# Performance work log

Measured on AMD Instinct MI355X. Metric: run time of the kernel, lower is better.

## Reference

```python
import jax, jax.numpy as jnp
import numpy as np

N_NODES = 100000
DIM = 256
N_SAMPLES = 64
N_CLASSES = 10


def setup_inputs() -> dict:
    key = jax.random.key(0)
    k1, k2, k3 = jax.random.split(key, 3)
    data = jax.random.normal(k1, (N_SAMPLES, DIM), dtype=jnp.float32)
    V = jax.random.uniform(k2, (N_NODES, DIM), dtype=jnp.float32)  # node matrix (torch.rand init)
    labels = jax.random.randint(k3, (N_SAMPLES,), 0, N_CLASSES)
    return {"data": data, "V": V, "labels": labels, "it": 0}


def reference(data, V, labels, it):
    # SOINN+ per-sample BMU search + BMU/sBMU weight pull, fixed node capacity.
    # eps schedules exactly as in ASOINN.forward.
    eps_b = 1.0 / (it + 2)
    eps_n = 1.0 / ((it + 1) * 100)

    def step(Vc, sample):
        # pairwise L2 distance of sample vs all nodes: [N]
        diff = sample[None, :] - Vc
        dists = jnp.sqrt(jnp.sum(diff * diff, axis=-1) + 1e-12)
        neg_vals, idx = jax.lax.top_k(-dists, 2)  # two smallest
        b, s = idx[0], idx[1]
        # update_bmu: V[b] += eps_b * (sample - V[b]); neighbor pull on sBMU
        Vc = Vc.at[b].add(eps_b * (sample - Vc[b]))
        Vc = Vc.at[s].add(eps_n * (sample - Vc[s]))
        return Vc, -neg_vals  # (b_dist, s_dist)

    V_final, bmu_dists = jax.lax.scan(step, V, data)
    return bmu_dists  # [N_SAMPLES, 2]
```

## Files before the change

kernel.cpp:

```cpp
#include <hip/hip_runtime.h>
#include <math.h>


#define N_NODES 100000
#define DIM     256
#define NS      64
#define NCH     1563
#define KC      32
#define NBMW    3125
#define CAP     4096
#define KL      192
#define KLS     136

typedef unsigned long long u64;

__device__ __forceinline__ u64 pk(float d, int i) {
  return ((u64)__float_as_uint(d) << 32) | (unsigned)i;
}
__device__ __forceinline__ u64 umin64(u64 a, u64 b) { return a < b ? a : b; }
__device__ __forceinline__ u64 umax64(u64 a, u64 b) { return a > b ? a : b; }
__device__ __forceinline__ void mrg2(u64& A0, u64& A1, u64 B0, u64 B1) {
  u64 m = umax64(A0, B0);
  A0 = umin64(A0, B0);
  A1 = umin64(umin64(A1, B1), m);
}

template <int C>
__device__ __forceinline__ u64 dpp64(u64 x) {
  unsigned lo = (unsigned)__builtin_amdgcn_update_dpp(
      (int)0xFFFFFFFF, (int)(unsigned)(x & 0xFFFFFFFFull), C, 0xF, 0xF, false);
  unsigned hi = (unsigned)__builtin_amdgcn_update_dpp(
      (int)0xFFFFFFFF, (int)(unsigned)(x >> 32), C, 0xF, 0xF, false);
  return ((u64)hi << 32) | lo;
}
template <int C>
__device__ __forceinline__ void dpp_round(u64& A0, u64& A1) {
  u64 B0 = dpp64<C>(A0);
  u64 B1 = dpp64<C>(A1);
  mrg2(A0, A1, B0, B1);
}

__global__ void k_xx(const float* __restrict__ X, float* __restrict__ XX) {
  int i = blockIdx.x, j = threadIdx.x;
  const float* xi = X + i * DIM;
  const float* xj = X + j * DIM;
  float acc = 0.f;
  for (int k = 0; k < DIM; k += 4) {
    float4 a = *(const float4*)(xi + k);
    float4 b = *(const float4*)(xj + k);
    acc += a.x * b.x + a.y * b.y + a.z * b.z + a.w * b.w;
  }
  XX[i * NS + j] = acc;
}

__global__ __launch_bounds__(256) void k_dist(const float* __restrict__ X,
                                              const float* __restrict__ V,
                                              const float* __restrict__ XX,
                                              float* __restrict__ P,
                                              float* __restrict__ PT,
                                              float* __restrict__ Q,
                                              u64* __restrict__ SUMC) {
  __shared__ float Xl[KC][68];
  __shared__ float Vl[KC][132];
  __shared__ float sq[128];
  const int tid = threadIdx.x;
  const int n0  = blockIdx.x * 128;
  const int ty  = tid >> 5;
  const int tx  = tid & 31;
  float acc[8][4];
#pragma unroll
  for (int i = 0; i < 8; i++)
#pragma unroll
    for (int u = 0; u < 4; u++) acc[i][u] = 0.f;
  float qa = 0.f;
  const int xsl = tid & 63;
  const int xkk = (tid >> 6) * 8;
  const int vn  = tid & 127;
  const int vkk = (tid >> 7) * 16;
  const bool vok = (n0 + vn < N_NODES);
  const float* vrow = V + (size_t)(n0 + vn) * DIM + vkk;
  const float* xrow = X + xsl * DIM + xkk;

  float4 xr0, xr1, vr[4];
  xr0 = *(const float4*)(xrow + 0);
  xr1 = *(const float4*)(xrow + 4);
#pragma unroll
  for (int m = 0; m < 4; m++)
    vr[m] = vok ? *(const float4*)(vrow + 4 * m) : make_float4(0.f, 0.f, 0.f, 0.f);

  for (int c = 0; c < 8; c++) {
    __syncthreads();
    Xl[xkk + 0][xsl] = xr0.x; Xl[xkk + 1][xsl] = xr0.y;
    Xl[xkk + 2][xsl] = xr0.z; Xl[xkk + 3][xsl] = xr0.w;
    Xl[xkk + 4][xsl] = xr1.x; Xl[xkk + 5][xsl] = xr1.y;
    Xl[xkk + 6][xsl] = xr1.z; Xl[xkk + 7][xsl] = xr1.w;
#pragma unroll
    for (int m = 0; m < 4; m++) {
      Vl[vkk + 4 * m + 0][vn] = vr[m].x; Vl[vkk + 4 * m + 1][vn] = vr[m].y;
      Vl[vkk + 4 * m + 2][vn] = vr[m].z; Vl[vkk + 4 * m + 3][vn] = vr[m].w;
    }
    __syncthreads();
    if (c + 1 < 8) {
      int kc = (c + 1) * KC;
      xr0 = *(const float4*)(xrow + kc);
      xr1 = *(const float4*)(xrow + kc + 4);
#pragma unroll
      for (int m = 0; m < 4; m++)
        vr[m] = vok ? *(const float4*)(vrow + kc + 4 * m)
                    : make_float4(0.f, 0.f, 0.f, 0.f);
    }
    if (tid < 128) {
      float qq = 0.f;
#pragma unroll 8
      for (int k = 0; k < KC; k++) { float t = Vl[k][tid]; qq += t * t; }
      qa += qq;
    }
#pragma unroll 4
    for (int k = 0; k < KC; k++) {
      float xs[8], vs[4];
      *(float4*)&xs[0] = *(const float4*)&Xl[k][ty * 8];
      *(float4*)&xs[4] = *(const float4*)&Xl[k][ty * 8 + 4];
      *(float4*)&vs[0] = *(const float4*)&Vl[k][tx * 4];
#pragma unroll
      for (int i = 0; i < 8; i++)
#pragma unroll
        for (int u = 0; u < 4; u++) acc[i][u] += xs[i] * vs[u];
    }
  }
  if (tid < 128) sq[tid] = qa;
  __syncthreads();
  if (tid < 128 && n0 + tid < N_NODES) Q[n0 + tid] = qa;
  float qs[4];
  *(float4*)&qs[0] = *(const float4*)&sq[tx * 4];
  const bool full = (n0 + 128) <= N_NODES;
#pragma unroll
  for (int i = 0; i < 8; i++) {
    int s = ty * 8 + i;
    float xn = XX[s * NS + s];
#pragma unroll
    for (int u = 0; u < 4; u++) acc[i][u] = xn - 2.f * acc[i][u] + qs[u];
    float* prow = P + (size_t)s * N_NODES + n0 + tx * 4;
    if (full) {
      *(float4*)(prow) = make_float4(acc[i][0], acc[i][1], acc[i][2], acc[i][3]);
    } else {
#pragma unroll
      for (int u = 0; u < 4; u++) {
        int n = n0 + tx * 4 + u;
        if (n < N_NODES) prow[u] = acc[i][u];
      }
    }
  }
#pragma unroll
  for (int u = 0; u < 4; u++) {
    int n = n0 + tx * 4 + u;
    if (n < N_NODES) {
      float* pt = PT + (size_t)n * NS + ty * 8;
      *(float4*)(pt)     = make_float4(acc[0][u], acc[1][u], acc[2][u], acc[3][u]);
      *(float4*)(pt + 4) = make_float4(acc[4][u], acc[5][u], acc[6][u], acc[7][u]);
    }
  }
#pragma unroll
  for (int i = 0; i < 8; i++) {
    int s = ty * 8 + i;
    u64 key = ~0ull;
#pragma unroll
    for (int u = 0; u < 4; u++) {
      int n = n0 + tx * 4 + u;
      if (n < N_NODES) key = umin64(key, pk(acc[i][u], n));
    }
#pragma unroll
    for (int off = 1; off <= 8; off <<= 1)
      key = umin64(key, (u64)__shfl_xor((unsigned long long)key, off, 64));
    if ((tx & 15) == 0) {
      int chunk = (n0 >> 6) + (tx >> 4);
      if (chunk < NCH) SUMC[(size_t)s * NCH + chunk] = key;
    }
  }
}

__global__ __launch_bounds__(1024) void k_build(const u64* __restrict__ SUMC,
                                                const float* __restrict__ P,
                                                u64* __restrict__ L) {
  __shared__ u64 A[CAP];
  __shared__ u64 Twave[16];
  __shared__ float Tsh;
  __shared__ int cnt;
  const int j = blockIdx.x, tid = threadIdx.x;
  const int w = tid >> 6, l = tid & 63;
  {
    int base = w * 98;
    u64 v0 = (base + l < NCH) ? SUMC[(size_t)j * NCH + base + l] : ~0ull;
    u64 v1 = (l < 34 && base + 64 + l < NCH)
                 ? SUMC[(size_t)j * NCH + base + 64 + l] : ~0ull;
    u64 s9 = ~0ull;
#pragma unroll
    for (int r = 0; r < 9; r++) {
      u64 m = umin64(v0, v1);
#pragma unroll
      for (int off = 1; off <= 32; off <<= 1)
        m = umin64(m, (u64)__shfl_xor((unsigned long long)m, off, 64));
      if (r == 8) { s9 = m; } else {
        if (v0 == m) v0 = ~0ull;
        if (v1 == m) v1 = ~0ull;
      }
    }
    if (l == 0) Twave[w] = s9;
  }
  __syncthreads();
  if (tid == 0) {
    u64 t = 0;
    for (int i = 0; i < 16; i++) t = umax64(t, Twave[i]);
    Tsh = __uint_as_float((unsigned)(t >> 32));
    cnt = 0;
  }
  __syncthreads();
  const float T = Tsh;
  const float* prow = P + (size_t)j * N_NODES;
  for (int n0 = tid * 4; n0 < N_NODES + 3; n0 += 4096) {
    float d[4];
    if (n0 + 3 < N_NODES) {
      float4 p = *(const float4*)(prow + n0);
      d[0] = p.x; d[1] = p.y; d[2] = p.z; d[3] = p.w;
    } else {
#pragma unroll
      for (int e = 0; e < 4; e++)
        d[e] = (n0 + e < N_NODES) ? prow[n0 + e] : INFINITY;
    }
#pragma unroll
    for (int e = 0; e < 4; e++) {
      if (d[e] <= T) {
        int pos = atomicAdd(&cnt, 1);
        if (pos < CAP) A[pos] = pk(d[e], n0 + e);
      }
    }
  }
  __syncthreads();
  int n = cnt; if (n > CAP) n = CAP;
  int M = 256; while (M < n) M <<= 1;
  for (int i = tid; i < M; i += 1024)
    if (i >= n) A[i] = ~0ull;
  __syncthreads();
  for (int k = 2; k <= M; k <<= 1)
    for (int s2 = k >> 1; s2 > 0; s2 >>= 1) {
      for (int i = tid; i < M; i += 1024) {
        int p = i ^ s2;
        if (p > i) {
          u64 a = A[i], b = A[p];
          bool up = ((i & k) == 0);
          if ((a > b) == up) { A[i] = b; A[p] = a; }
        }
      }
      __syncthreads();
    }
  for (int i = tid; i < KLS; i += 1024) L[(size_t)j * KL + i] = A[i];
}

__global__ __launch_bounds__(192) void k_seq(
    const float* __restrict__ PT, const float* __restrict__ Q,
    const float* __restrict__ XXg, const u64* __restrict__ L,
    const int* __restrict__ itp, float* __restrict__ out) {
  __shared__ float XXl[NS * 65];
  __shared__ float g[128][65];
  __shared__ float qv[128];
  __shared__ unsigned int bitmap[NBMW];
  __shared__ int tracked[128];
  __shared__ u64 cand16[NS][16];
  __shared__ float specg[4][6][NS];
  __shared__ float specq[4][6];
  __shared__ int   specid[4][6];
  __shared__ int ready[NS];
  __shared__ int done[NS];

  const int tid = threadIdx.x;
  const int wv = tid >> 6;
  const int lane = tid & 63;

  for (int i = tid; i < NS * NS; i += 192) {
    int r = i >> 6, c = i & 63;
    XXl[r * 65 + c] = XXg[i];
  }
  for (int i = tid; i < NBMW; i += 192) bitmap[i] = 0u;
  for (int i = tid; i < NS; i += 192) { ready[i] = 0; done[i] = 0; }
  __syncthreads();

  const int it = itp[0];
  const float eps_b = 1.0f / (float)(it + 2);
  const float eps_n = 1.0f / (float)((it + 1) * 100);
  const float xdl = XXl[lane * 65 + lane];

  if (wv == 0) {
    int ns = 0;
    int pw0 = -1, pw1 = -1, pw2 = -1, pw3 = -1;
    for (int j = 0; j < NS; j++) {
      while (__hip_atomic_load(&ready[j], __ATOMIC_ACQUIRE,
                               __HIP_MEMORY_SCOPE_WORKGROUP) == 0)
        __builtin_amdgcn_s_sleep(1);
      const int sb = j & 3;
      u64 ck = (lane < 16) ? cand16[j][lane] : ~0ull;
      float sgv[6], sqv[6]; int sid[6];
#pragma unroll
      for (int s = 0; s < 6; s++) {
        sgv[s] = specg[sb][s][lane];
        sid[s] = specid[sb][s];
        sqv[s] = specq[sb][s];
      }
      float gA = g[lane][j], gB = g[lane + 64][j];
      float qvA = qv[lane],  qvB = qv[lane + 64];
      int   tA = tracked[lane], tB = tracked[lane + 64];
      float xrow = XXl[j * 65 + lane];
      float xnj  = XXl[j * 65 + j];
      u64 A0 = ~0ull, A1 = ~0ull;
      {
        int id = (int)(unsigned)(ck & 0xFFFFFFFFull);
        bool ok = (ck != ~0ull) && id != pw0 && id != pw1 && id != pw2 && id != pw3;
        if (ok) { A0 = ck; }
      }
      if (lane < ns)      { float d = xnj - 2.f * gA + qvA; mrg2(A0, A1, pk(d, tA), ~0ull); }
      if (lane + 64 < ns) { float d = xnj - 2.f * gB + qvB; mrg2(A0, A1, pk(d, tB), ~0ull); }
      dpp_round<0x111>(A0, A1);
      dpp_round<0x112>(A0, A1);
      dpp_round<0x114>(A0, A1);
      dpp_round<0x118>(A0, A1);
      dpp_round<0x142>(A0, A1);
      dpp_round<0x143>(A0, A1);
      const int r0 = (int)(unsigned)__builtin_amdgcn_readlane(
          (int)(unsigned)(A0 & 0xFFFFFFFFull), 63);
      const int r1 = (int)(unsigned)__builtin_amdgcn_readlane(
          (int)(unsigned)(A1 & 0xFFFFFFFFull), 63);
      if (lane == 63) {
        float2 o;
        o.x = sqrtf(fmaxf(__uint_as_float((unsigned)(A0 >> 32)), 0.f) + 1e-12f);
        o.y = sqrtf(fmaxf(__uint_as_float((unsigned)(A1 >> 32)), 0.f) + 1e-12f);
        *(float2*)(out + j * 2) = o;
      }
      bool h0a = (lane < ns) && (tA == r0);
      bool h0b = (lane + 64 < ns) && (tB == r0);
      u64 mk0a = __ballot(h0a), mk0b = __ballot(h0b);
      bool new0 = (mk0a | mk0b) == 0ull;
      int sl0 = new0 ? ns
                     : (mk0a ? (__ffsll((unsigned long long)mk0a) - 1)
                             : (64 + __ffsll((unsigned long long)mk0b) - 1));
      bool h1a = (lane < ns) && (tA == r1);
      bool h1b = (lane + 64 < ns) && (tB == r1);
      u64 mk1a = __ballot(h1a), mk1b = __ballot(h1b);
      bool new1 = (mk1a | mk1b) == 0ull;
      int sl1 = new1 ? (ns + (new0 ? 1 : 0))
                     : (mk1a ? (__ffsll((unsigned long long)mk1a) - 1)
                             : (64 + __ffsll((unsigned long long)mk1b) - 1));
      bool hit0 = false, hit1 = false;
      float pv0 = 0.f, qq0 = 0.f, pv1 = 0.f, qq1 = 0.f;
#pragma unroll
      for (int s = 0; s < 6; s++) {
        bool h0 = (sid[s] == r0), h1 = (sid[s] == r1);
        pv0 = h0 ? sgv[s] : pv0;  qq0 = h0 ? sqv[s] : qq0;  hit0 |= h0;
        pv1 = h1 ? sgv[s] : pv1;  qq1 = h1 ? sqv[s] : qq1;  hit1 |= h1;
      }
      if (new0 && !hit0) { pv0 = PT[(size_t)r0 * NS + lane]; qq0 = Q[r0]; }
      if (new1 && !hit1) { pv1 = PT[(size_t)r1 * NS + lane]; qq1 = Q[r1]; }
      float gt0 = g[sl0][lane];
      float gt1 = g[sl1][lane];
      float gold0 = new0 ? (0.5f * (xdl + qq0 - pv0)) : gt0;
      float qold0 = new0 ? qq0
                         : __uint_as_float((unsigned)__builtin_amdgcn_readlane(
                               (int)__float_as_uint(sl0 < 64 ? qvA : qvB), sl0 & 63));
      float gj0 = __uint_as_float(
          (unsigned)__builtin_amdgcn_readlane((int)__float_as_uint(gold0), j));
      g[sl0][lane] = (1.f - eps_b) * gold0 + eps_b * xrow;
      if (lane == 0) {
        float om = 1.f - eps_b;
        qv[sl0] = om * om * qold0 + 2.f * eps_b * om * gj0 + eps_b * eps_b * xnj;
        tracked[sl0] = r0;
        if (new0) bitmap[r0 >> 5] |= 1u << (r0 & 31);
      }
      float gold1 = new1 ? (0.5f * (xdl + qq1 - pv1)) : gt1;
      float qold1 = new1 ? qq1
                         : __uint_as_float((unsigned)__builtin_amdgcn_readlane(
                               (int)__float_as_uint(sl1 < 64 ? qvA : qvB), sl1 & 63));
      float gj1 = __uint_as_float(
          (unsigned)__builtin_amdgcn_readlane((int)__float_as_uint(gold1), j));
      g[sl1][lane] = (1.f - eps_n) * gold1 + eps_n * xrow;
      if (lane == 0) {
        float on = 1.f - eps_n;
        qv[sl1] = on * on * qold1 + 2.f * eps_n * on * gj1 + eps_n * eps_n * xnj;
        tracked[sl1] = r1;
        if (new1) bitmap[r1 >> 5] |= 1u << (r1 & 31);
      }
      ns += (new0 ? 1 : 0) + (new1 ? 1 : 0);
      pw2 = pw0; pw3 = pw1; pw0 = r0; pw1 = r1;
      __hip_atomic_store(&done[j], 1, __ATOMIC_RELEASE,
                         __HIP_MEMORY_SCOPE_WORKGROUP);
    }
  } else {
    for (int t = (wv == 1 ? 0 : 1); t < NS; t += 2) {
      if (t >= 3) {
        while (__hip_atomic_load(&done[t - 3], __ATOMIC_ACQUIRE,
                                 __HIP_MEMORY_SCOPE_WORKGROUP) == 0)
          __builtin_amdgcn_s_sleep(1);
      }
      const u64* Lr = L + (size_t)t * KL;
      u64 e0 = Lr[lane], e1 = Lr[lane + 64];
      u64 e2 = (lane < 8) ? Lr[128 + lane] : ~0ull;
      int i0 = (int)(unsigned)(e0 & 0xFFFFFFFFull);
      int i1 = (int)(unsigned)(e1 & 0xFFFFFFFFull);
      int i2 = (int)(unsigned)(e2 & 0xFFFFFFFFull);
      bool t0 = (e0 == ~0ull) || ((bitmap[i0 >> 5] >> (i0 & 31)) & 1u);
      bool t1 = (e1 == ~0ull) || ((bitmap[i1 >> 5] >> (i1 & 31)) & 1u);
      bool t2 = (e2 == ~0ull) || ((bitmap[i2 >> 5] >> (i2 & 31)) & 1u);
      u64 um0 = ~__ballot(t0), um1 = ~__ballot(t1), um2 = ~__ballot(t2);
      u64 below = (1ull << lane) - 1;
      int c0n = __popcll((unsigned long long)um0);
      int c1n = __popcll((unsigned long long)um1);
      int rank0 = __popcll((unsigned long long)(um0 & below));
      int rank1 = c0n + __popcll((unsigned long long)(um1 & below));
      int rank2 = c0n + c1n + __popcll((unsigned long long)(um2 & below));
      if (!t0 && rank0 < 16) cand16[t][rank0] = e0;
      if (!t1 && rank1 < 16) cand16[t][rank1] = e1;
      if (!t2 && rank2 < 16) cand16[t][rank2] = e2;
      int U = c0n + c1n + __popcll((unsigned long long)um2);
      if (lane < 16 && lane >= U) cand16[t][lane] = ~0ull;
      const int sb = t & 3;
      int ids[6];
#pragma unroll
      for (int s = 0; s < 6; s++)
        ids[s] = (int)(unsigned)(cand16[t][s] & 0xFFFFFFFFull);
#pragma unroll
      for (int s = 0; s < 6; s++)
        specg[sb][s][lane] = PT[(size_t)ids[s] * NS + lane];
      if (lane < 6) {
        specid[sb][lane] = ids[lane];
        specq[sb][lane] = Q[ids[lane]];
      }
      __hip_atomic_store(&ready[t], 1, __ATOMIC_RELEASE,
                         __HIP_MEMORY_SCOPE_WORKGROUP);
    }
  }
}

extern "C" void kernel_launch(void* const* d_in, const int* in_sizes, int n_in,
                              void* d_out, int out_size, void* d_ws, size_t ws_size,
                              hipStream_t stream) {
  const float* X  = (const float*)d_in[0];
  const float* V  = (const float*)d_in[1];
  const int*  itp = (const int*)d_in[3];
  float* out = (float*)d_out;

  char* ws = (char*)d_ws;
  size_t off = 0;
  auto alloc = [&](size_t bytes) -> void* {
    size_t o = (off + 255) & ~(size_t)255;
    off = o + bytes;
    return (void*)(ws + o);
  };
  float* P    = (float*)alloc((size_t)NS * N_NODES * sizeof(float));
  float* PT   = (float*)alloc((size_t)NS * N_NODES * sizeof(float));
  float* Q    = (float*)alloc((size_t)N_NODES * sizeof(float));
  float* XXp  = (float*)alloc((size_t)NS * NS * sizeof(float));
  u64*   SUMC = (u64*)alloc((size_t)NS * NCH * sizeof(u64));
  u64*   Lst  = (u64*)alloc((size_t)NS * KL * sizeof(u64));

  k_xx   <<<NS, NS, 0, stream>>>(X, XXp);
  k_dist <<<(N_NODES + 127) / 128, 256, 0, stream>>>(X, V, XXp, P, PT, Q, SUMC);
  k_build<<<NS, 1024, 0, stream>>>(SUMC, P, Lst);
  k_seq  <<<1, 192, 0, stream>>>(PT, Q, XXp, Lst, itp, out);
}
```

Baseline: 310.2 us.

## Split ready flag, encode tracked slot in key, prefetch candidate list early

The single ready flag becomes two: one signals that the candidate list is published and one signals that the speculative PT rows are loaded. The sequential wave can then start its argmin reduction before the speculative gathers finish. Tracked entries now carry their slot index and a 'tracked' bit in the packed key, so the slot and the new/old status come directly from the reduction result instead of four ballots plus ffs. Helper waves also issue their global loads of the candidate list before waiting on the done flag. Together these shorten the serial critical path, at the cost of an extra spin-wait and the assumption that node ids fit in 17 bits.

Result: no change. 308.1 us (-0.7%).

```diff
diff --git a/kernel.cpp b/kernel.cpp
--- a/kernel.cpp
+++ b/kernel.cpp
@@ -16,6 +16,10 @@
 
 __device__ __forceinline__ u64 pk(float d, int i) {
   return ((u64)__float_as_uint(d) << 32) | (unsigned)i;
+}
+__device__ __forceinline__ u64 tkey(float d, int slot, int node) {
+  return ((u64)__float_as_uint(d) << 32) |
+         (u64)(0x80000000u | ((unsigned)slot << 17) | (unsigned)node);
 }
 __device__ __forceinline__ u64 umin64(u64 a, u64 b) { return a < b ? a : b; }
 __device__ __forceinline__ u64 umax64(u64 a, u64 b) { return a > b ? a : b; }
@@ -268,7 +272,8 @@
   __shared__ float specg[4][6][NS];
   __shared__ float specq[4][6];
   __shared__ int   specid[4][6];
-  __shared__ int ready[NS];
+  __shared__ int readyC[NS];
+  __shared__ int readyS[NS];
   __shared__ int done[NS];
 
   const int tid = threadIdx.x;
@@ -280,7 +285,7 @@
     XXl[r * 65 + c] = XXg[i];
   }
   for (int i = tid; i < NBMW; i += 192) bitmap[i] = 0u;
-  for (int i = tid; i < NS; i += 192) { ready[i] = 0; done[i] = 0; }
+  for (int i = tid; i < NS; i += 192) { readyC[i] = 0; readyS[i] = 0; done[i] = 0; }
   __syncthreads();
 
   const int it = itp[0];
@@ -292,18 +297,11 @@
     int ns = 0;
     int pw0 = -1, pw1 = -1, pw2 = -1, pw3 = -1;
     for (int j = 0; j < NS; j++) {
-      while (__hip_atomic_load(&ready[j], __ATOMIC_ACQUIRE,
+      while (__hip_atomic_load(&readyC[j], __ATOMIC_ACQUIRE,
                                __HIP_MEMORY_SCOPE_WORKGROUP) == 0)
         __builtin_amdgcn_s_sleep(1);
       const int sb = j & 3;
       u64 ck = (lane < 16) ? cand16[j][lane] : ~0ull;
-      float sgv[6], sqv[6]; int sid[6];
-#pragma unroll
-      for (int s = 0; s < 6; s++) {
-        sgv[s] = specg[sb][s][lane];
-        sid[s] = specid[sb][s];
-        sqv[s] = specq[sb][s];
-      }
       float gA = g[lane][j], gB = g[lane + 64][j];
       float qvA = qv[lane],  qvB = qv[lane + 64];
       int   tA = tracked[lane], tB = tracked[lane + 64];
@@ -315,38 +313,42 @@
         bool ok = (ck != ~0ull) && id != pw0 && id != pw1 && id != pw2 && id != pw3;
         if (ok) { A0 = ck; }
       }
-      if (lane < ns)      { float d = xnj - 2.f * gA + qvA; mrg2(A0, A1, pk(d, tA), ~0ull); }
-      if (lane + 64 < ns) { float d = xnj - 2.f * gB + qvB; mrg2(A0, A1, pk(d, tB), ~0ull); }
+      if (lane < ns)      { float d = xnj - 2.f * gA + qvA; mrg2(A0, A1, tkey(d, lane, tA), ~0ull); }
+      if (lane + 64 < ns) { float d = xnj - 2.f * gB + qvB; mrg2(A0, A1, tkey(d, lane + 64, tB), ~0ull); }
       dpp_round<0x111>(A0, A1);
       dpp_round<0x112>(A0, A1);
       dpp_round<0x114>(A0, A1);
       dpp_round<0x118>(A0, A1);
       dpp_round<0x142>(A0, A1);
       dpp_round<0x143>(A0, A1);
-      const int r0 = (int)(unsigned)__builtin_amdgcn_readlane(
+      const unsigned lo0 = (unsigned)__builtin_amdgcn_readlane(
           (int)(unsigned)(A0 & 0xFFFFFFFFull), 63);
-      const int r1 = (int)(unsigned)__builtin_amdgcn_readlane(
+      const unsigned lo1 = (unsigned)__builtin_amdgcn_readlane(
           (int)(unsigned)(A1 & 0xFFFFFFFFull), 63);
+      const int r0 = (int)(lo0 & 0x1FFFFu);
+      const int r1 = (int)(lo1 & 0x1FFFFu);
+      const bool new0 = (lo0 & 0x80000000u) == 0u;
+      const bool new1 = (lo1 & 0x80000000u) == 0u;
+      const int sl0 = new0 ? ns : (int)((lo0 >> 17) & 127u);
+      const int sl1 = new1 ? (ns + (new0 ? 1 : 0)) : (int)((lo1 >> 17) & 127u);
       if (lane == 63) {
         float2 o;
         o.x = sqrtf(fmaxf(__uint_as_float((unsigned)(A0 >> 32)), 0.f) + 1e-12f);
         o.y = sqrtf(fmaxf(__uint_as_float((unsigned)(A1 >> 32)), 0.f) + 1e-12f);
         *(float2*)(out + j * 2) = o;
       }
-      bool h0a = (lane < ns) && (tA == r0);
-      bool h0b = (lane + 64 < ns) && (tB == r0);
-      u64 mk0a = __ballot(h0a), mk0b = __ballot(h0b);
-      bool new0 = (mk0a | mk0b) == 0ull;
-      int sl0 = new0 ? ns
-                     : (mk0a ? (__ffsll((unsigned long long)mk0a) - 1)
-                             : (64 + __ffsll((unsigned long long)mk0b) - 1));
-      bool h1a = (lane < ns) && (tA == r1);
-      bool h1b = (lane + 64 < ns) && (tB == r1);
-      u64 mk1a = __ballot(h1a), mk1b = __ballot(h1b);
-      bool new1 = (mk1a | mk1b) == 0ull;
-      int sl1 = new1 ? (ns + (new0 ? 1 : 0))
-                     : (mk1a ? (__ffsll((unsigned long long)mk1a) - 1)
-                             : (64 + __ffsll((unsigned long long)mk1b) - 1));
+      float gt0 = g[sl0][lane];
+      float gt1 = g[sl1][lane];
+      while (__hip_atomic_load(&readyS[j], __ATOMIC_ACQUIRE,
+                               __HIP_MEMORY_SCOPE_WORKGROUP) == 0)
+        __builtin_amdgcn_s_sleep(1);
+      float sgv[6], sqv[6]; int sid[6];
+#pragma unroll
+      for (int s = 0; s < 6; s++) {
+        sgv[s] = specg[sb][s][lane];
+        sid[s] = specid[sb][s];
+        sqv[s] = specq[sb][s];
+      }
       bool hit0 = false, hit1 = false;
       float pv0 = 0.f, qq0 = 0.f, pv1 = 0.f, qq1 = 0.f;
 #pragma unroll
@@ -357,8 +359,6 @@
       }
       if (new0 && !hit0) { pv0 = PT[(size_t)r0 * NS + lane]; qq0 = Q[r0]; }
       if (new1 && !hit1) { pv1 = PT[(size_t)r1 * NS + lane]; qq1 = Q[r1]; }
-      float gt0 = g[sl0][lane];
-      float gt1 = g[sl1][lane];
       float gold0 = new0 ? (0.5f * (xdl + qq0 - pv0)) : gt0;
       float qold0 = new0 ? qq0
                          : __uint_as_float((unsigned)__builtin_amdgcn_readlane(
@@ -392,14 +392,14 @@
     }
   } else {
     for (int t = (wv == 1 ? 0 : 1); t < NS; t += 2) {
+      const u64* Lr = L + (size_t)t * KL;
+      u64 e0 = Lr[lane], e1 = Lr[lane + 64];
+      u64 e2 = (lane < 8) ? Lr[128 + lane] : ~0ull;
       if (t >= 3) {
         while (__hip_atomic_load(&done[t - 3], __ATOMIC_ACQUIRE,
                                  __HIP_MEMORY_SCOPE_WORKGROUP) == 0)
           __builtin_amdgcn_s_sleep(1);
       }
-      const u64* Lr = L + (size_t)t * KL;
-      u64 e0 = Lr[lane], e1 = Lr[lane + 64];
-      u64 e2 = (lane < 8) ? Lr[128 + lane] : ~0ull;
       int i0 = (int)(unsigned)(e0 & 0xFFFFFFFFull);
       int i1 = (int)(unsigned)(e1 & 0xFFFFFFFFull);
       int i2 = (int)(unsigned)(e2 & 0xFFFFFFFFull);
@@ -418,6 +418,8 @@
       if (!t2 && rank2 < 16) cand16[t][rank2] = e2;
       int U = c0n + c1n + __popcll((unsigned long long)um2);
       if (lane < 16 && lane >= U) cand16[t][lane] = ~0ull;
+      __hip_atomic_store(&readyC[t], 1, __ATOMIC_RELEASE,
+                         __HIP_MEMORY_SCOPE_WORKGROUP);
       const int sb = t & 3;
       int ids[6];
 #pragma unroll
@@ -430,7 +432,7 @@
         specid[sb][lane] = ids[lane];
         specq[sb][lane] = Q[ids[lane]];
       }
-      __hip_atomic_store(&ready[t], 1, __ATOMIC_RELEASE,
+      __hip_atomic_store(&readyS[t], 1, __ATOMIC_RELEASE,
                          __HIP_MEMORY_SCOPE_WORKGROUP);
     }
   }
```
